# Optimization experiments

Hardware: AMD Instinct MI355X
Metric: run time of the kernel (lower is better)

## Reference

```python
import jax, jax.numpy as jnp
import numpy as np

DIM_MSA = 256
DIM_PAIR = 128
DIM_HID = 32
EPS = 0.001
LN_EPS = 1e-5


def setup_inputs() -> dict:
    key = jax.random.key(0)
    ks = jax.random.split(key, 8)
    b, m, n = 1, 256, 384
    x = jax.random.normal(ks[0], (b, m, n, DIM_MSA), dtype=jnp.float32)
    mask = jax.random.randint(ks[1], (b, m, n), 0, 2).astype(jnp.int32)
    ln_g = jnp.ones((DIM_MSA,), jnp.float32)
    ln_b = jnp.zeros((DIM_MSA,), jnp.float32)
    s = 1.0 / np.sqrt(DIM_MSA)
    wl = jax.random.normal(ks[2], (DIM_MSA, DIM_HID), jnp.float32) * s
    bl = jnp.zeros((DIM_HID,), jnp.float32)
    wr = jax.random.normal(ks[3], (DIM_MSA, DIM_HID), jnp.float32) * s
    br = jnp.zeros((DIM_HID,), jnp.float32)
    wo = jax.random.normal(ks[4], (DIM_HID * DIM_HID, DIM_PAIR), jnp.float32) / np.sqrt(DIM_HID * DIM_HID)
    bo = jnp.zeros((DIM_PAIR,), jnp.float32)
    return {"x": x, "mask": mask, "ln_g": ln_g, "ln_b": ln_b,
            "wl": wl, "bl": bl, "wr": wr, "br": br, "wo": wo, "bo": bo}


def reference(x, mask, ln_g, ln_b, wl, bl, wr, br, wo, bo):
    # LayerNorm over last dim
    mu = jnp.mean(x, axis=-1, keepdims=True)
    var = jnp.mean(jnp.square(x - mu), axis=-1, keepdims=True)
    xn = (x - mu) * jax.lax.rsqrt(var + LN_EPS) * ln_g + ln_b
    left = xn @ wl + bl    # [b,m,n,c]
    right = xn @ wr + br   # [b,m,n,d]
    m = mask.astype(x.dtype)  # 0/1 mask [b,m,n]
    left = left * m[..., None]
    right = right * m[..., None]
    # masked outer-product sum over MSA dim m, no 6D materialization
    outer = jnp.einsum('bmic,bmjd->bijcd', left, right)
    b_, i_, j_ = outer.shape[0], outer.shape[1], outer.shape[2]
    outer = outer.reshape(b_, i_, j_, DIM_HID * DIM_HID)
    out = outer @ wo + bo  # [b,i,j,pairwise]
    cnt = jnp.einsum('bmi,bmj->bij', m, m)  # valid-pair counts
    return out / (cnt[..., None] + EPS)
```

## Files before the change

### kernel.cpp

```cpp
#include <hip/hip_runtime.h>
#include <hip/hip_bf16.h>
#include <stdint.h>


typedef float f32x4 __attribute__((ext_vector_type(4)));
typedef __bf16 bf16x8 __attribute__((ext_vector_type(8)));
typedef __bf16 bf16x4 __attribute__((ext_vector_type(4)));

#define NSEQ 384
#define NMSA 256

typedef const __attribute__((address_space(1))) unsigned int* gptr_t;
typedef __attribute__((address_space(3))) unsigned int* lptr_t;

__device__ __forceinline__ void gload_lds16(const void* g, void* l) {
    __builtin_amdgcn_global_load_lds((gptr_t)g, (lptr_t)l, 16, 0, 0);
}

__global__ __launch_bounds__(256) void prep_all_kernel(
    const float* __restrict__ wo,
    const float* __restrict__ wl, const float* __restrict__ wr,
    const float* __restrict__ bl, const float* __restrict__ br,
    const float* __restrict__ ln_g, const float* __restrict__ ln_b,
    const int* __restrict__ mask,
    __bf16* __restrict__ woT, __bf16* __restrict__ wg,
    float* __restrict__ Gc, float* __restrict__ B2,
    float* __restrict__ inv_cnt)
{
    const int blk = blockIdx.x;
    __shared__ int mi[NMSA];
    __shared__ float sg[4], sb[4];

    if (blk < 512) {
        int gid = blk * 256 + threadIdx.x;
        int p = gid >> 10, q = gid & 1023;
        int d = q >> 5, c = q & 31;
        woT[gid] = (__bf16)wo[(c * 32 + d) * 128 + p];
    } else if (blk < 576) {
        const int c = blk - 512;
        const int k = threadIdx.x;
        float w = (c < 32) ? wl[k * 32 + c] : wr[k * 32 + (c - 32)];
        __bf16 wgb = (__bf16)(w * ln_g[k]);
        wg[c * 256 + k] = wgb;
        float gsum = (float)wgb;
        float bsum = w * ln_b[k];
        for (int off = 32; off; off >>= 1) {
            gsum += __shfl_down(gsum, off);
            bsum += __shfl_down(bsum, off);
        }
        int wid = k >> 6, lane = k & 63;
        if (lane == 0) { sg[wid] = gsum; sb[wid] = bsum; }
        __syncthreads();
        if (k == 0) {
            Gc[c] = sg[0] + sg[1] + sg[2] + sg[3];
            B2[c] = sb[0] + sb[1] + sb[2] + sb[3] + ((c < 32) ? bl[c] : br[c - 32]);
        }
    } else {
        const int i = blk - 576;
        const int t = threadIdx.x;
        mi[t] = mask[t * NSEQ + i];
        __syncthreads();
        for (int j = t; j < NSEQ; j += 256) {
            int acc = 0;
            for (int m = 0; m < NMSA; ++m)
                acc += mi[m] & mask[m * NSEQ + j];
            inv_cnt[i * NSEQ + j] = 1.0f / ((float)acc + 0.001f);
        }
    }
}

__global__ __launch_bounds__(256) void ln_proj_kernel(
    const float* __restrict__ x, const int* __restrict__ mask,
    const __bf16* __restrict__ wg, const float* __restrict__ Gc,
    const float* __restrict__ B2,
    __bf16* __restrict__ leftT, __bf16* __restrict__ rightT)
{
    const int n = blockIdx.x % NSEQ;
    const int mh = blockIdx.x / NSEQ;
    const int m0 = mh * 128;
    const int tid = threadIdx.x;
    __shared__ __bf16 xnT[128 * 40];
    __shared__ float muS[128], rsS[128], maskS[128], GcS[64], B2S[64];

    if (tid < 64) { GcS[tid] = Gc[tid]; B2S[tid] = B2[tid]; }
    if (tid < 128) maskS[tid] = (float)mask[(m0 + tid) * NSEQ + n];

    const int wid = tid >> 6, lane = tid & 63;
    const int lhi = lane >> 4, llo = lane & 15;
    const int wrq = wid >> 1, wcq = wid & 1;
    float ps[4] = {}, pq[4] = {};
    f32x4 acc[2][4] = {};

    for (int k0 = 0; k0 < 256; k0 += 32) {
        #pragma unroll
        for (int cc = 0; cc < 4; ++cc) {
            int ch = tid + cc * 256;
            int mR = ch >> 3, c4 = ch & 7;
            f32x4 v = *reinterpret_cast<const f32x4*>(x + ((size_t)(m0 + mR) * NSEQ + n) * 256 + k0 + c4 * 4);
            ps[cc] += v[0] + v[1] + v[2] + v[3];
            pq[cc] += v[0]*v[0] + v[1]*v[1] + v[2]*v[2] + v[3]*v[3];
            __bf16* dst = xnT + mR * 40 + c4 * 4;
            dst[0] = (__bf16)v[0]; dst[1] = (__bf16)v[1];
            dst[2] = (__bf16)v[2]; dst[3] = (__bf16)v[3];
        }
        __syncthreads();
        bf16x8 af[2], bfr[4];
        #pragma unroll
        for (int fr = 0; fr < 2; ++fr)
            af[fr] = *reinterpret_cast<const bf16x8*>(wg + (size_t)(wrq * 32 + fr * 16 + llo) * 256 + k0 + lhi * 8);
        #pragma unroll
        for (int fc = 0; fc < 4; ++fc)
            bfr[fc] = *reinterpret_cast<const bf16x8*>(xnT + (wcq * 64 + fc * 16 + llo) * 40 + lhi * 8);
        #pragma unroll
        for (int fr = 0; fr < 2; ++fr)
            #pragma unroll
            for (int fc = 0; fc < 4; ++fc)
                acc[fr][fc] = __builtin_amdgcn_mfma_f32_16x16x32_bf16(af[fr], bfr[fc], acc[fr][fc], 0, 0, 0);
        __syncthreads();
    }

    #pragma unroll
    for (int cc = 0; cc < 4; ++cc) {
        float s = ps[cc], q = pq[cc];
        s += __shfl_xor(s, 1); q += __shfl_xor(q, 1);
        s += __shfl_xor(s, 2); q += __shfl_xor(q, 2);
        s += __shfl_xor(s, 4); q += __shfl_xor(q, 4);
        if ((tid & 7) == 0) {
            int mR = (tid >> 3) + cc * 32;
            float mu = s * (1.f / 256.f);
            float var = q * (1.f / 256.f) - mu * mu;
            muS[mR] = mu;
            rsS[mR] = rsqrtf(var + 1e-5f);
        }
    }
    __syncthreads();

    #pragma unroll
    for (int fr = 0; fr < 2; ++fr) {
        #pragma unroll
        for (int fc = 0; fc < 4; ++fc) {
            int mR = wcq * 64 + fc * 16 + llo;
            float mv = maskS[mR], rs = rsS[mR], mu = muS[mR];
            #pragma unroll
            for (int r = 0; r < 4; ++r) {
                int c = wrq * 32 + fr * 16 + lhi * 4 + r;
                float val = (acc[fr][fc][r] - mu * GcS[c]) * rs + B2S[c];
                __bf16 bv = (__bf16)(val * mv);
                if (c < 32) leftT [(size_t)(n * 32 + c)        * 256 + m0 + mR] = bv;
                else        rightT[(size_t)(n * 32 + (c - 32)) * 256 + m0 + mR] = bv;
            }
        }
    }
}

__global__ __launch_bounds__(512, 2) void outer_gemm_kernel(
    const __bf16* __restrict__ leftT, const __bf16* __restrict__ rightT,
    const __bf16* __restrict__ woT, const float* __restrict__ bo,
    const float* __restrict__ inv_cnt, float* __restrict__ out)
{
    __shared__ char smem[131072];
    const int tid = threadIdx.x;
    const int wid = tid >> 6, lane = tid & 63;
    const int lhi = lane >> 4, llo = lane & 15;
    const int wr = wid >> 2, wc = wid & 3;

    int wg_ = blockIdx.x;
    int xcd = wg_ & 7;
    int g   = wg_ >> 3;
    int big = g / 48;
    int rem = g - big * 48;
    int bjx = rem >> 3;
    int bii = rem & 7;
    int bi  = big * 8 + bii;
    int bj  = xcd * 6 + bjx;

    char* Abuf[2] = { smem,         smem + 65536 };
    char* Bbuf[2] = { smem + 32768, smem + 98304 };

    auto STAGE = [&](int buf, int k0) {
        #pragma unroll
        for (int it = 0; it < 4; ++it) {
            int q = it * 512 + wid * 64 + lane;
            int r = q >> 3;
            int s = (q & 7) ^ (r & 7);
            int ldsoff = (it * 512 + wid * 64) * 16;
            gload_lds16(leftT  + (size_t)(bi * 256 + r) * 256 + k0 + s * 8, Abuf[buf] + ldsoff);
            gload_lds16(rightT + (size_t)(bj * 256 + r) * 256 + k0 + s * 8, Bbuf[buf] + ldsoff);
        }
    };

    f32x4 acc[8][4] = {};

    STAGE(0, 0);
    #pragma unroll
    for (int t = 0; t < 4; ++t) {
        if (t < 3) {
            STAGE((t + 1) & 1, (t + 1) * 64);
            asm volatile("s_waitcnt vmcnt(8)" ::: "memory");
        } else {
            asm volatile("s_waitcnt vmcnt(0)" ::: "memory");
        }
        __builtin_amdgcn_s_barrier();
        const __bf16* Al = (const __bf16*)Abuf[t & 1];
        const __bf16* Bl = (const __bf16*)Bbuf[t & 1];
        #pragma unroll
        for (int kk = 0; kk < 2; ++kk) {
            bf16x8 af[8], bfv[4];
            int sb = kk * 4 + lhi;
            #pragma unroll
            for (int fr = 0; fr < 8; ++fr) {
                int row = wr * 128 + fr * 16 + llo;
                af[fr] = *(const bf16x8*)(Al + row * 64 + ((sb ^ (row & 7)) << 3));
            }
            #pragma unroll
            for (int fc = 0; fc < 4; ++fc) {
                int row = wc * 64 + fc * 16 + llo;
                bfv[fc] = *(const bf16x8*)(Bl + row * 64 + ((sb ^ (row & 7)) << 3));
            }
            asm volatile("s_waitcnt lgkmcnt(0)" ::: "memory");
            __builtin_amdgcn_sched_barrier(0);
            __builtin_amdgcn_s_setprio(1);
            #pragma unroll
            for (int fr = 0; fr < 8; ++fr)
                #pragma unroll
                for (int fc = 0; fc < 4; ++fc)
                    acc[fr][fc] = __builtin_amdgcn_mfma_f32_16x16x32_bf16(af[fr], bfv[fc], acc[fr][fc], 0, 0, 0);
            __builtin_amdgcn_s_setprio(0);
            __builtin_amdgcn_s_barrier();
        }
    }

    __bf16* Aep = (__bf16*)smem;
    #pragma unroll
    for (int fr = 0; fr < 8; ++fr) {
        #pragma unroll
        for (int fc = 0; fc < 4; ++fc) {
            int ij = (wr * 4 + (fr >> 1)) * 8 + wc * 2 + (fc >> 1);
            int t = ((fc & 1) * 16 + llo) * 4 + (fr & 1) * 2 + (lhi >> 1);
            int phys = (((t & 3) << 5) | (t >> 2)) ^ (ij & 15);
            bf16x4 v;
            v[0] = (__bf16)acc[fr][fc][0]; v[1] = (__bf16)acc[fr][fc][1];
            v[2] = (__bf16)acc[fr][fc][2]; v[3] = (__bf16)acc[fr][fc][3];
            *(bf16x4*)(Aep + ij * 1024 + (phys << 3) + (lhi & 1) * 4) = v;
        }
    }
    __syncthreads();

    f32x4 eacc[4] = {};
    const int p = wid * 16 + llo;
    const __bf16* wrow = woT + (size_t)p * 1024 + lhi * 8;
    #pragma unroll 8
    for (int k0 = 0; k0 < 1024; k0 += 32) {
        bf16x8 bw = *(const bf16x8*)(wrow + k0);
        int base = (lhi << 5) | (k0 >> 5);
        #pragma unroll
        for (int mf = 0; mf < 4; ++mf) {
            int ij = mf * 16 + llo;
            int phys = base ^ llo;
            bf16x8 a = *(const bf16x8*)(Aep + ij * 1024 + (phys << 3));
            eacc[mf] = __builtin_amdgcn_mfma_f32_16x16x32_bf16(a, bw, eacc[mf], 0, 0, 0);
        }
    }

    const float bov = bo[p];
    #pragma unroll
    for (int mf = 0; mf < 4; ++mf) {
        #pragma unroll
        for (int r = 0; r < 4; ++r) {
            int ij = mf * 16 + lhi * 4 + r;
            int i = bi * 8 + (ij >> 3);
            int j = bj * 8 + (ij & 7);
            size_t idx = (size_t)i * NSEQ + j;
            out[idx * 128 + p] = (eacc[mf][r] + bov) * inv_cnt[idx];
        }
    }
}

extern "C" void kernel_launch(void* const* d_in, const int* in_sizes, int n_in,
                              void* d_out, int out_size, void* d_ws, size_t ws_size,
                              hipStream_t stream) {
    const float* x    = (const float*)d_in[0];
    const int*   mask = (const int*)  d_in[1];
    const float* ln_g = (const float*)d_in[2];
    const float* ln_b = (const float*)d_in[3];
    const float* wl   = (const float*)d_in[4];
    const float* bl   = (const float*)d_in[5];
    const float* wr   = (const float*)d_in[6];
    const float* br   = (const float*)d_in[7];
    const float* wo   = (const float*)d_in[8];
    const float* bo   = (const float*)d_in[9];
    float* out = (float*)d_out;

    char* ws = (char*)d_ws;
    __bf16* leftT   = (__bf16*)(ws);
    __bf16* rightT  = (__bf16*)(ws + 6291456);
    __bf16* woT     = (__bf16*)(ws + 12582912);
    __bf16* wg      = (__bf16*)(ws + 12845056);
    float*  Gc      = (float*) (ws + 12877824);
    float*  B2      = (float*) (ws + 12878080);
    float*  inv_cnt = (float*) (ws + 12878336);

    prep_all_kernel<<<960, 256, 0, stream>>>(wo, wl, wr, bl, br, ln_g, ln_b, mask,
                                             woT, wg, Gc, B2, inv_cnt);
    ln_proj_kernel<<<768, 256, 0, stream>>>(x, mask, wg, Gc, B2, leftT, rightT);
    outer_gemm_kernel<<<2304, 512, 0, stream>>>(leftT, rightT, woT, bo, inv_cnt, out);
}
```

Baseline: 187.7 us.

## Compute pair counts via bitpacked mask popcount and halve LN-proj tile

```diff
diff --git a/kernel.cpp b/kernel.cpp
--- a/kernel.cpp
+++ b/kernel.cpp
@@ -25,11 +25,9 @@
     const int* __restrict__ mask,
     __bf16* __restrict__ woT, __bf16* __restrict__ wg,
     float* __restrict__ Gc, float* __restrict__ B2,
-    float* __restrict__ inv_cnt)
+    unsigned long long* __restrict__ maskbits)
 {
     const int blk = blockIdx.x;
-    __shared__ int mi[NMSA];
-    __shared__ float sg[4], sb[4];
 
     if (blk < 512) {
         int gid = blk * 256 + threadIdx.x;
@@ -37,6 +35,7 @@
         int d = q >> 5, c = q & 31;
         woT[gid] = (__bf16)wo[(c * 32 + d) * 128 + p];
     } else if (blk < 576) {
+        __shared__ float sg[4], sb[4];
         const int c = blk - 512;
         const int k = threadIdx.x;
         float w = (c < 32) ? wl[k * 32 + c] : wr[k * 32 + (c - 32)];
@@ -56,15 +55,20 @@
             B2[c] = sb[0] + sb[1] + sb[2] + sb[3] + ((c < 32) ? bl[c] : br[c - 32]);
         }
     } else {
-        const int i = blk - 576;
-        const int t = threadIdx.x;
-        mi[t] = mask[t * NSEQ + i];
+        __shared__ int tile[256 * 65];
+        const int b = blk - 576;
+        const int tid = threadIdx.x;
+        #pragma unroll
+        for (int it = 0; it < 64; ++it) {
+            int e = it * 256 + tid;
+            int m = e >> 6, c = e & 63;
+            tile[m * 65 + c] = mask[m * NSEQ + b * 64 + c];
+        }
         __syncthreads();
-        for (int j = t; j < NSEQ; j += 256) {
-            int acc = 0;
-            for (int m = 0; m < NMSA; ++m)
-                acc += mi[m] & mask[m * NSEQ + j];
-            inv_cnt[i * NSEQ + j] = 1.0f / ((float)acc + 0.001f);
+        const int w = tid >> 6, lane = tid & 63;
+        for (int c = 0; c < 64; ++c) {
+            unsigned long long bits = __ballot(tile[(w * 64 + lane) * 65 + c] != 0);
+            if (lane == 0) maskbits[(size_t)(b * 64 + c) * 4 + w] = bits;
         }
     }
 }
@@ -73,27 +77,51 @@
     const float* __restrict__ x, const int* __restrict__ mask,
     const __bf16* __restrict__ wg, const float* __restrict__ Gc,
     const float* __restrict__ B2,
-    __bf16* __restrict__ leftT, __bf16* __restrict__ rightT)
+    const unsigned long long* __restrict__ maskbits,
+    __bf16* __restrict__ leftT, __bf16* __restrict__ rightT,
+    float* __restrict__ inv_cnt)
 {
+    const int tid = threadIdx.x;
+
+    if (blockIdx.x >= 1536) {
+        const int idx = blockIdx.x - 1536;
+        const int w = tid >> 6, lane = tid & 63;
+        const int i = idx * 4 + w;
+        unsigned long long bi0 = maskbits[(size_t)i * 4 + 0];
+        unsigned long long bi1 = maskbits[(size_t)i * 4 + 1];
+        unsigned long long bi2 = maskbits[(size_t)i * 4 + 2];
+        unsigned long long bi3 = maskbits[(size_t)i * 4 + 3];
+        #pragma unroll
+        for (int s = 0; s < 6; ++s) {
+            int j = lane + s * 64;
+            const unsigned long long* bj = maskbits + (size_t)j * 4;
+            int c = __popcll(bi0 & bj[0]) + __popcll(bi1 & bj[1])
+                  + __popcll(bi2 & bj[2]) + __popcll(bi3 & bj[3]);
+            inv_cnt[i * NSEQ + j] = 1.0f / ((float)c + 0.001f);
+        }
+        return;
+    }
+
     const int n = blockIdx.x % NSEQ;
     const int mh = blockIdx.x / NSEQ;
-    const int m0 = mh * 128;
-    const int tid = threadIdx.x;
-    __shared__ __bf16 xnT[128 * 40];
-    __shared__ float muS[128], rsS[128], maskS[128], GcS[64], B2S[64];
-
-    if (tid < 64) { GcS[tid] = Gc[tid]; B2S[tid] = B2[tid]; }
-    if (tid < 128) maskS[tid] = (float)mask[(m0 + tid) * NSEQ + n];
+    const int m0 = mh * 64;
+    __shared__ __bf16 xnT[64 * 40];
+    __shared__ float muS[64], rsS[64], maskS[64], GcS[64], B2S[64];
+
+    if (tid < 64) {
+        GcS[tid] = Gc[tid]; B2S[tid] = B2[tid];
+        maskS[tid] = (float)mask[(m0 + tid) * NSEQ + n];
+    }
 
     const int wid = tid >> 6, lane = tid & 63;
     const int lhi = lane >> 4, llo = lane & 15;
     const int wrq = wid >> 1, wcq = wid & 1;
-    float ps[4] = {}, pq[4] = {};
-    f32x4 acc[2][4] = {};
+    float ps[2] = {}, pq[2] = {};
+    f32x4 acc[2][2] = {};
 
     for (int k0 = 0; k0 < 256; k0 += 32) {
         #pragma unroll
-        for (int cc = 0; cc < 4; ++cc) {
+        for (int cc = 0; cc < 2; ++cc) {
             int ch = tid + cc * 256;
             int mR = ch >> 3, c4 = ch & 7;
             f32x4 v = *reinterpret_cast<const f32x4*>(x + ((size_t)(m0 + mR) * NSEQ + n) * 256 + k0 + c4 * 4);
@@ -104,23 +132,23 @@
             dst[2] = (__bf16)v[2]; dst[3] = (__bf16)v[3];
         }
         __syncthreads();
-        bf16x8 af[2], bfr[4];
+        bf16x8 af[2], bfr[2];
         #pragma unroll
         for (int fr = 0; fr < 2; ++fr)
             af[fr] = *reinterpret_cast<const bf16x8*>(wg + (size_t)(wrq * 32 + fr * 16 + llo) * 256 + k0 + lhi * 8);
         #pragma unroll
-        for (int fc = 0; fc < 4; ++fc)
-            bfr[fc] = *reinterpret_cast<const bf16x8*>(xnT + (wcq * 64 + fc * 16 + llo) * 40 + lhi * 8);
+        for (int fc = 0; fc < 2; ++fc)
+            bfr[fc] = *reinterpret_cast<const bf16x8*>(xnT + (wcq * 32 + fc * 16 + llo) * 40 + lhi * 8);
         #pragma unroll
         for (int fr = 0; fr < 2; ++fr)
             #pragma unroll
-            for (int fc = 0; fc < 4; ++fc)
+            for (int fc = 0; fc < 2; ++fc)
                 acc[fr][fc] = __builtin_amdgcn_mfma_f32_16x16x32_bf16(af[fr], bfr[fc], acc[fr][fc], 0, 0, 0);
         __syncthreads();
     }
 
     #pragma unroll
-    for (int cc = 0; cc < 4; ++cc) {
+    for (int cc = 0; cc < 2; ++cc) {
         float s = ps[cc], q = pq[cc];
         s += __shfl_xor(s, 1); q += __shfl_xor(q, 1);
         s += __shfl_xor(s, 2); q += __shfl_xor(q, 2);
@@ -138,8 +166,8 @@
     #pragma unroll
     for (int fr = 0; fr < 2; ++fr) {
         #pragma unroll
-        for (int fc = 0; fc < 4; ++fc) {
-            int mR = wcq * 64 + fc * 16 + llo;
+        for (int fc = 0; fc < 2; ++fc) {
+            int mR = wcq * 32 + fc * 16 + llo;
             float mv = maskS[mR], rs = rsS[mR], mu = muS[mR];
             #pragma unroll
             for (int r = 0; r < 4; ++r) {
@@ -299,9 +327,11 @@
     float*  Gc      = (float*) (ws + 12877824);
     float*  B2      = (float*) (ws + 12878080);
     float*  inv_cnt = (float*) (ws + 12878336);
-
-    prep_all_kernel<<<960, 256, 0, stream>>>(wo, wl, wr, bl, br, ln_g, ln_b, mask,
-                                             woT, wg, Gc, B2, inv_cnt);
-    ln_proj_kernel<<<768, 256, 0, stream>>>(x, mask, wg, Gc, B2, leftT, rightT);
+    unsigned long long* maskbits = (unsigned long long*)(ws + 13468160);
+
+    prep_all_kernel<<<582, 256, 0, stream>>>(wo, wl, wr, bl, br, ln_g, ln_b, mask,
+                                             woT, wg, Gc, B2, maskbits);
+    ln_proj_kernel<<<1632, 256, 0, stream>>>(x, mask, wg, Gc, B2, maskbits,
+                                             leftT, rightT, inv_cnt);
     outer_gemm_kernel<<<2304, 512, 0, stream>>>(leftT, rightT, woT, bo, inv_cnt, out);
 }
```

Measured after the change: 176.9 us. -5.8%, faster.
